# Optimization experiments

Hardware: AMD Instinct MI355X
Metric: run time of the kernel (lower is better)

## Reference

```python
import jax, jax.numpy as jnp
import numpy as np

N, C, H, W = 2, 128, 64, 64
N_HEAD = 4
GROUPS = 16
EPS = 1e-5


def group_norm(x, scale, offset):
    # haiku GroupNorm, channels_first: normalize over (channels-in-group, h, w)
    n, c, h, w = x.shape
    xg = x.reshape(n, GROUPS, c // GROUPS, h, w)
    mu = xg.mean(axis=(2, 3, 4), keepdims=True)
    var = xg.var(axis=(2, 3, 4), keepdims=True)
    xg = (xg - mu) * jax.lax.rsqrt(var + EPS)
    return xg.reshape(n, c, h, w) * scale[None, :, None, None] + offset[None, :, None, None]


def setup_inputs() -> dict:
    key = jax.random.key(0)
    ks = jax.random.split(key, 4)
    inv_sqrt_c = 1.0 / np.sqrt(C).astype(np.float32)
    return {
        "x": jax.random.normal(ks[0], (N, C, H, W), dtype=jnp.float32),
        "w_qkv": jax.random.normal(ks[1], (C, 3 * C), dtype=jnp.float32) * inv_sqrt_c,
        "b_qkv": jnp.zeros((3 * C,), dtype=jnp.float32),
        "w_out": jax.random.normal(ks[2], (C, C), dtype=jnp.float32) * inv_sqrt_c,
        "b_out": jnp.zeros((C,), dtype=jnp.float32),
        "gn1_scale": jnp.ones((C,), dtype=jnp.float32),
        "gn1_offset": jnp.zeros((C,), dtype=jnp.float32),
        "gn2_scale": jnp.ones((C,), dtype=jnp.float32),
        "gn2_offset": jnp.zeros((C,), dtype=jnp.float32),
    }


def reference(x, w_qkv, b_qkv, w_out, b_out, gn1_scale, gn1_offset, gn2_scale, gn2_offset):
    n, c, h, w = x.shape
    dh = c // N_HEAD
    # GroupNorm (x is reassigned, so the residual uses the normalized x)
    xn = group_norm(x, gn1_scale, gn1_offset)
    # 1x1 conv qkv projection: [n, 3c, h, w]
    qkv = jnp.einsum('nchw,cd->ndhw', xn, w_qkv) + b_qkv[None, :, None, None]
    # [n, 3H, dh, hw] -> [n, 3H, hw, dh]
    qkv = jnp.swapaxes(qkv.reshape(n, N_HEAD * 3, dh, h * w), 2, 3)
    q, k, v = jnp.split(qkv, 3, axis=1)  # each [n, H, hw, dh]
    scale = dh ** (-0.25)
    # [n, H, hw, hw] attention matrix (the memory-bound core)
    att = jax.nn.softmax((q * scale) @ (jnp.swapaxes(k, 2, 3) * scale), axis=3)
    y = jnp.swapaxes(att @ v, 2, 3).reshape(n, c, h, w)
    # 1x1 conv out projection + GroupNorm + residual
    out = jnp.einsum('nchw,cd->ndhw', y, w_out) + b_out[None, :, None, None]
    return xn + group_norm(out, gn2_scale, gn2_offset)
```

## Files before the change

kernel.cpp:

```cpp
#include <hip/hip_runtime.h>
#include <hip/hip_bf16.h>
#include <math.h>

constexpr int cHW   = 4096;
constexpr int cC    = 128;
constexpr int cNH   = 4;
constexpr int cDH   = 32;
constexpr float cEPS = 1e-5f;
constexpr float cQS = 0.2550347805f;
constexpr int SPLIT = 4;

typedef short bh8 __attribute__((ext_vector_type(8)));
typedef float f4  __attribute__((ext_vector_type(4)));

static __device__ __forceinline__ unsigned short f2bf(float f) {
  union { __hip_bfloat16 h; unsigned short u; } cv;
  cv.h = __float2bfloat16(f);
  return cv.u;
}
static __device__ __forceinline__ unsigned pack2bf(float a, float b) {
  return (unsigned)f2bf(a) | ((unsigned)f2bf(b) << 16);
}
static __device__ __forceinline__ unsigned pack_trunc(float a, float b) {
  unsigned ua = __builtin_bit_cast(unsigned, a);
  unsigned ub = __builtin_bit_cast(unsigned, b);
  return (ua >> 16) | (ub & 0xffff0000u);
}
static __device__ __forceinline__ float bflo(unsigned pk) {
  return __builtin_bit_cast(float, pk << 16);
}
static __device__ __forceinline__ float bfhi(unsigned pk) {
  return __builtin_bit_cast(float, pk & 0xffff0000u);
}

__device__ __forceinline__ void block_reduce2(float& a, float& b, float* sbuf) {
  #pragma unroll
  for (int off = 32; off > 0; off >>= 1) {
    a += __shfl_down(a, off, 64);
    b += __shfl_down(b, off, 64);
  }
  int wave = threadIdx.x >> 6;
  int lane = threadIdx.x & 63;
  if (lane == 0) { sbuf[wave] = a; sbuf[4 + wave] = b; }
  __syncthreads();
  if (threadIdx.x == 0) {
    sbuf[8] = sbuf[0] + sbuf[1] + sbuf[2] + sbuf[3];
    sbuf[9] = sbuf[4] + sbuf[5] + sbuf[6] + sbuf[7];
  }
  __syncthreads();
  a = sbuf[8];
  b = sbuf[9];
}

__global__ __launch_bounds__(256)
void prep(const float* __restrict__ x, float* __restrict__ part,
          const float* __restrict__ wq, const float* __restrict__ wo,
          unsigned short* __restrict__ wqT, unsigned short* __restrict__ woT) {
  __shared__ float lds[32 * 133];
  int L = threadIdx.x;
  if (blockIdx.x < 256) {
    int ng = blockIdx.x >> 3, sl = blockIdx.x & 7;
    const float4* s4 = (const float4*)x;
    float s = 0.f, s2 = 0.f;
    #pragma unroll
    for (int i = 0; i < 4; i++) {
      int idx = i * 256 + L;
      int c = idx >> 7, tt = idx & 127;
      float4 v = s4[(size_t)(ng * 8 + c) * 1024 + sl * 128 + tt];
      s  += v.x + v.y + v.z + v.w;
      s2 += v.x*v.x + v.y*v.y + v.z*v.z + v.w*v.w;
    }
    block_reduce2(s, s2, lds);
    if (L == 0) { part[blockIdx.x * 2] = s; part[blockIdx.x * 2 + 1] = s2; }
  } else {
    int bx = blockIdx.x - 256;
    const float* src; unsigned short* dst; int W, d0;
    if (bx < 12) { src = wq; dst = wqT; W = 384; d0 = bx * 32; }
    else         { src = wo; dst = woT; W = 128; d0 = (bx - 12) * 32; }
    #pragma unroll
    for (int i = 0; i < 16; i++) {
      int c = i * 8 + (L >> 5), d = L & 31;
      lds[d * 133 + c] = src[(size_t)c * W + d0 + d];
    }
    __syncthreads();
    int d = L >> 3, ch = L & 7, c0 = ch * 16;
    unsigned pk[8];
    #pragma unroll
    for (int j = 0; j < 8; j++)
      pk[j] = pack2bf(lds[d * 133 + c0 + 2 * j], lds[d * 133 + c0 + 2 * j + 1]);
    uint4* d4 = (uint4*)(dst + (size_t)(d0 + d) * 128 + c0);
    d4[0] = make_uint4(pk[0], pk[1], pk[2], pk[3]);
    d4[1] = make_uint4(pk[4], pk[5], pk[6], pk[7]);
  }
}

__global__ __launch_bounds__(256)
void gn_stats(const float* __restrict__ src, float* __restrict__ part) {
  __shared__ float sbuf[10];
  int ng = blockIdx.x >> 3, sl = blockIdx.x & 7;
  const float4* s4 = (const float4*)src;
  float s = 0.f, s2 = 0.f;
  #pragma unroll
  for (int i = 0; i < 4; i++) {
    int idx = i * 256 + threadIdx.x;
    int c = idx >> 7, tt = idx & 127;
    float4 v = s4[(size_t)(ng * 8 + c) * 1024 + sl * 128 + tt];
    s  += v.x + v.y + v.z + v.w;
    s2 += v.x*v.x + v.y*v.y + v.z*v.z + v.w*v.w;
  }
  block_reduce2(s, s2, sbuf);
  if (threadIdx.x == 0) { part[blockIdx.x * 2] = s; part[blockIdx.x * 2 + 1] = s2; }
}

__global__ __launch_bounds__(256)
void gn1_pack(const float* __restrict__ x, const float* __restrict__ part,
              const float* __restrict__ sc, const float* __restrict__ of,
              unsigned short* __restrict__ xnB) {
  int cc = blockIdx.x, ts = blockIdx.y, n = blockIdx.z;
  int ng = n * 16 + cc;
  float s = 0.f, s2 = 0.f;
  #pragma unroll
  for (int p = 0; p < 8; p++) { s += part[(ng*8+p)*2]; s2 += part[(ng*8+p)*2+1]; }
  float mu = s * (1.0f / 32768.0f);
  float rinv = rsqrtf(s2 * (1.0f / 32768.0f) - mu * mu + cEPS);
  int t = ts * 256 + threadIdx.x;
  float v[8];
  #pragma unroll
  for (int j = 0; j < 8; j++) {
    int c = cc * 8 + j;
    float a = rinv * sc[c];
    float bo = of[c] - mu * a;
    v[j] = x[((size_t)n * cC + c) * cHW + t] * a + bo;
  }
  unsigned pk[4];
  #pragma unroll
  for (int j = 0; j < 4; j++) pk[j] = pack2bf(v[2*j], v[2*j+1]);
  ((uint4*)xnB)[(size_t)(n * 16 + cc) * cHW + t] = make_uint4(pk[0], pk[1], pk[2], pk[3]);
}

__global__ __launch_bounds__(256)
void qkv_mfma(const unsigned short* __restrict__ xnB, const unsigned short* __restrict__ wqT,
              const float* __restrict__ bq, unsigned* __restrict__ qB,
              unsigned* __restrict__ kB, unsigned* __restrict__ vI) {
  __shared__ float vbuf[64 * 36];
  const int L = threadIdx.x & 63, w = threadIdx.x >> 6;
  const int c16 = L & 15, q = L >> 4;
  const int t0 = blockIdx.x * 64, dg = blockIdx.y, n = blockIdx.z;
  const int nh = n * 4 + (dg & 3), d0 = dg * 32;
  const f4 zf = {0.f, 0.f, 0.f, 0.f};
  f4 acc0 = zf, acc1 = zf;
  const int trow = t0 + w * 16 + c16;
  #pragma unroll
  for (int ks = 0; ks < 4; ks++) {
    bh8 a  = *(const bh8*)(xnB + ((size_t)(n * 16 + ks * 4 + q) * cHW + trow) * 8);
    bh8 b0 = *(const bh8*)(wqT + (size_t)(d0 + c16) * 128 + ks * 32 + q * 8);
    bh8 b1 = *(const bh8*)(wqT + (size_t)(d0 + 16 + c16) * 128 + ks * 32 + q * 8);
    acc0 = __builtin_amdgcn_mfma_f32_16x16x32_bf16(a, b0, acc0, 0, 0, 0);
    acc1 = __builtin_amdgcn_mfma_f32_16x16x32_bf16(a, b1, acc1, 0, 0, 0);
  }
  float blo = bq[d0 + c16], bhi = bq[d0 + 16 + c16];
  if (dg < 8) {
    float scl = (dg < 4) ? cQS : 1.0f;
    unsigned* dst = (dg < 4) ? qB : kB;
    #pragma unroll
    for (int r = 0; r < 4; r++) {
      unsigned pk = pack2bf((acc0[r] + blo) * scl, (acc1[r] + bhi) * scl);
      dst[((size_t)nh * cHW + t0 + w * 16 + q * 4 + r) * 16 + c16] = pk;
    }
  } else {
    #pragma unroll
    for (int r = 0; r < 4; r++) {
      vbuf[(w * 16 + q * 4 + r) * 36 + c16]      = acc0[r] + blo;
      vbuf[(w * 16 + q * 4 + r) * 36 + 16 + c16] = acc1[r] + bhi;
    }
    __syncthreads();
    int t16 = threadIdx.x & 15, dh8 = (threadIdx.x >> 4) & 15;
    #pragma unroll
    for (int blk = 0; blk < 2; blk++)
      #pragma unroll
      for (int hh = 0; hh < 2; hh++) {
        int dh = dh8 + hh * 16;
        float lo = vbuf[(blk * 32 + t16) * 36 + dh];
        float hi = vbuf[(blk * 32 + 16 + t16) * 36 + dh];
        vI[((size_t)nh * 32 + dh) * 2048 + (size_t)(t0 / 32 + blk) * 16 + t16] = pack2bf(lo, hi);
      }
  }
}

__global__ __launch_bounds__(256)
void flash_mfma(const unsigned short* __restrict__ qB,
                const unsigned short* __restrict__ kB,
                const unsigned short* __restrict__ vI,
                unsigned* __restrict__ opart, float* __restrict__ lpart) {
  __shared__ float pbuf[4][1280];
  const int w = threadIdx.x >> 6, L = threadIdx.x & 63;
  const int c16 = L & 15, q = L >> 4;
  const int qt = blockIdx.x * 4 + w, nh = blockIdx.y, ph = blockIdx.z;
  float* pb = pbuf[w];
  const f4 zf = {0.f, 0.f, 0.f, 0.f};
  const short oneb = 0x3F80;
  const bh8 ones = {oneb, oneb, oneb, oneb, oneb, oneb, oneb, oneb};

  const unsigned short* qb = qB + ((size_t)nh * cHW + qt * 32) * cDH;
  bh8 qa[2];
  qa[0] = *(const bh8*)(qb + (size_t)c16 * cDH + q * 8);
  qa[1] = *(const bh8*)(qb + (size_t)(16 + c16) * cDH + q * 8);

  f4 o[2][2] = {{zf, zf}, {zf, zf}};
  f4 lacc[2] = {zf, zf};

  const unsigned short* kb = kB + (size_t)nh * cHW * cDH;
  const unsigned short* vb = vI + (size_t)nh * cDH * cHW;

  const int kbeg = ph * (cHW / SPLIT);
  const int kend = kbeg + cHW / SPLIT;

  for (int kt = kbeg; kt < kend; kt += 64) {
    bh8 kf[4];
    #pragma unroll
    for (int s = 0; s < 4; s++)
      kf[s] = *(const bh8*)(kb + (size_t)(kt + s*16 + c16) * cDH + q * 8);
    bh8 vf[2][2];
    #pragma unroll
    for (int ks = 0; ks < 2; ks++)
      #pragma unroll
      for (int dt = 0; dt < 2; dt++)
        vf[ks][dt] = *(const bh8*)(vb + (size_t)(dt*16 + c16) * cHW + kt + ks*32 + q*8);

    f4 sf[2][4];
    #pragma unroll
    for (int rt = 0; rt < 2; rt++)
      #pragma unroll
      for (int s = 0; s < 4; s++)
        sf[rt][s] = __builtin_amdgcn_mfma_f32_16x16x32_bf16(qa[rt], kf[s], zf, 0, 0, 0);

    #pragma unroll
    for (int rt = 0; rt < 2; rt++) {
      #pragma unroll
      for (int s = 0; s < 4; s++)
        #pragma unroll
        for (int r = 0; r < 4; r++)
          sf[rt][s][r] = __builtin_amdgcn_exp2f(sf[rt][s][r]);
      #pragma unroll
      for (int st = 0; st < 2; st++)
        #pragma unroll
        for (int r = 0; r < 4; r++) {
          unsigned pk = pack_trunc(sf[rt][2*st][r], sf[rt][2*st+1][r]);
          pb[(rt*2 + st)*320 + (q*4 + r)*20 + c16] = __builtin_bit_cast(float, pk);
        }
    }
    #pragma unroll
    for (int rt = 0; rt < 2; rt++)
      #pragma unroll
      for (int st = 0; st < 2; st++) {
        bh8 pa = *(const bh8*)(pb + (rt*2 + st)*320 + c16*20 + q*4);
        o[rt][0] = __builtin_amdgcn_mfma_f32_16x16x32_bf16(pa, vf[st][0], o[rt][0], 0, 0, 0);
        o[rt][1] = __builtin_amdgcn_mfma_f32_16x16x32_bf16(pa, vf[st][1], o[rt][1], 0, 0, 0);
        lacc[rt] = __builtin_amdgcn_mfma_f32_16x16x32_bf16(pa, ones, lacc[rt], 0, 0, 0);
      }
  }

  size_t base_r = (size_t)ph * 32768 + (size_t)nh * cHW + (size_t)qt * 32;
  #pragma unroll
  for (int rt = 0; rt < 2; rt++)
    #pragma unroll
    for (int r = 0; r < 4; r++) {
      size_t rr = base_r + rt*16 + q*4 + r;
      if (c16 == 0) lpart[rr] = lacc[rt][r];
      opart[rr * 16 + c16] = pack_trunc(o[rt][0][r], o[rt][1][r]);
    }
}

__global__ __launch_bounds__(256)
void combine(const unsigned* __restrict__ opart, const float* __restrict__ lpart,
             unsigned* __restrict__ yB) {
  size_t r = (size_t)blockIdx.x * 256 + threadIdx.x;
  float l = 0.f;
  #pragma unroll
  for (int p = 0; p < SPLIT; p++) l += lpart[(size_t)p * 32768 + r];
  float e[32];
  #pragma unroll
  for (int j = 0; j < 32; j++) e[j] = 0.f;
  #pragma unroll
  for (int p = 0; p < SPLIT; p++) {
    const uint4* op = (const uint4*)(opart + ((size_t)p * 32768 + r) * 16);
    #pragma unroll
    for (int j = 0; j < 4; j++) {
      uint4 v = op[j];
      e[j*4+0] += bflo(v.x); e[16+j*4+0] += bfhi(v.x);
      e[j*4+1] += bflo(v.y); e[16+j*4+1] += bfhi(v.y);
      e[j*4+2] += bflo(v.z); e[16+j*4+2] += bfhi(v.z);
      e[j*4+3] += bflo(v.w); e[16+j*4+3] += bfhi(v.w);
    }
  }
  float inv = 1.0f / l;
  unsigned pk[16];
  #pragma unroll
  for (int m = 0; m < 16; m++) pk[m] = pack2bf(e[2*m] * inv, e[2*m+1] * inv);
  uint4* dst = (uint4*)(yB + r * 16);
  #pragma unroll
  for (int j = 0; j < 4; j++)
    dst[j] = make_uint4(pk[4*j], pk[4*j+1], pk[4*j+2], pk[4*j+3]);
}

__global__ __launch_bounds__(256)
void out_mfma(const unsigned short* __restrict__ yB, const unsigned short* __restrict__ woT,
              const float* __restrict__ bo, float* __restrict__ proj) {
  __shared__ float obuf[64 * 36];
  const int L = threadIdx.x & 63, w = threadIdx.x >> 6;
  const int c16 = L & 15, q = L >> 4;
  const int t0 = blockIdx.x * 64, d0 = blockIdx.y * 32, n = blockIdx.z;
  const f4 zf = {0.f, 0.f, 0.f, 0.f};
  f4 acc0 = zf, acc1 = zf;
  const int trow = t0 + w * 16 + c16;
  #pragma unroll
  for (int h = 0; h < 4; h++) {
    bh8 a  = *(const bh8*)(yB + ((size_t)(n * 4 + h) * cHW + trow) * 32 + q * 8);
    bh8 b0 = *(const bh8*)(woT + (size_t)(d0 + c16) * 128 + h * 32 + q * 8);
    bh8 b1 = *(const bh8*)(woT + (size_t)(d0 + 16 + c16) * 128 + h * 32 + q * 8);
    acc0 = __builtin_amdgcn_mfma_f32_16x16x32_bf16(a, b0, acc0, 0, 0, 0);
    acc1 = __builtin_amdgcn_mfma_f32_16x16x32_bf16(a, b1, acc1, 0, 0, 0);
  }
  float blo = bo[d0 + c16], bhi = bo[d0 + 16 + c16];
  #pragma unroll
  for (int r = 0; r < 4; r++) {
    obuf[(w * 16 + q * 4 + r) * 36 + c16]      = acc0[r] + blo;
    obuf[(w * 16 + q * 4 + r) * 36 + 16 + c16] = acc1[r] + bhi;
  }
  __syncthreads();
  int t16 = threadIdx.x & 15, d8 = (threadIdx.x >> 4) & 15;
  #pragma unroll
  for (int tc = 0; tc < 4; tc++)
    #pragma unroll
    for (int hh = 0; hh < 2; hh++) {
      int d = d8 + hh * 16;
      proj[((size_t)n * cC + d0 + d) * cHW + t0 + tc * 16 + t16] =
          obuf[(tc * 16 + t16) * 36 + d];
    }
}

__global__ __launch_bounds__(256)
void gn2_apply(const float* __restrict__ x, const float* __restrict__ proj,
               const float* __restrict__ p1, const float* __restrict__ p2,
               const float* __restrict__ s1, const float* __restrict__ o1,
               const float* __restrict__ s2, const float* __restrict__ o2,
               float* __restrict__ out) {
  int tid = blockIdx.x * 256 + threadIdx.x;
  int Cg = tid >> 8;
  int n = Cg >> 7, ch = Cg & 127, g = ch >> 3, ng = n * 16 + g;
  float sa = 0.f, sb = 0.f, ta = 0.f, tb = 0.f;
  #pragma unroll
  for (int p = 0; p < 8; p++) {
    sa += p1[(ng*8+p)*2]; sb += p1[(ng*8+p)*2+1];
    ta += p2[(ng*8+p)*2]; tb += p2[(ng*8+p)*2+1];
  }
  float mu1 = sa * (1.0f/32768.0f);
  float ri1 = rsqrtf(sb * (1.0f/32768.0f) - mu1*mu1 + cEPS);
  float a1 = ri1 * s1[ch], b1 = o1[ch] - mu1 * a1;
  float mu2 = ta * (1.0f/32768.0f);
  float ri2 = rsqrtf(tb * (1.0f/32768.0f) - mu2*mu2 + cEPS);
  float a2 = ri2 * s2[ch], b2 = o2[ch] - mu2 * a2;
  const float4* x4 = (const float4*)x;
  const float4* pr4 = (const float4*)proj;
  float4* o4 = (float4*)out;
  #pragma unroll
  for (int i = 0; i < 4; i++) {
    size_t f = (size_t)tid * 4 + i;
    float4 xv = x4[f], pv = pr4[f];
    float4 r;
    r.x = xv.x * a1 + b1 + pv.x * a2 + b2;
    r.y = xv.y * a1 + b1 + pv.y * a2 + b2;
    r.z = xv.z * a1 + b1 + pv.z * a2 + b2;
    r.w = xv.w * a1 + b1 + pv.w * a2 + b2;
    o4[f] = r;
  }
}

extern "C" void kernel_launch(void* const* d_in, const int* in_sizes, int n_in,
                              void* d_out, int out_size, void* d_ws, size_t ws_size,
                              hipStream_t stream) {
  const float* x     = (const float*)d_in[0];
  const float* w_qkv = (const float*)d_in[1];
  const float* b_qkv = (const float*)d_in[2];
  const float* w_out = (const float*)d_in[3];
  const float* b_out = (const float*)d_in[4];
  const float* g1s   = (const float*)d_in[5];
  const float* g1o   = (const float*)d_in[6];
  const float* g2s   = (const float*)d_in[7];
  const float* g2o   = (const float*)d_in[8];
  float* out = (float*)d_out;
  float* ws  = (float*)d_ws;

  const size_t MAP = (size_t)2 * cC * cHW;
  float* proj    = ws;
  float* lpart   = proj + MAP;
  float* stats1  = lpart + (size_t)SPLIT * 32768;
  float* stats2  = stats1 + 512;
  unsigned* opart = (unsigned*)(stats2 + 512);
  unsigned* qB   = opart + (size_t)SPLIT * 32768 * 16;
  unsigned* kB   = qB + MAP / 2;
  unsigned* vI   = kB + MAP / 2;
  unsigned* yB   = vI + MAP / 2;
  unsigned short* xnB = (unsigned short*)(yB + MAP / 2);
  unsigned short* wqT = xnB + MAP;
  unsigned short* woT = wqT + 49152;

  prep      <<<dim3(272),           256, 0, stream>>>(x, stats1, w_qkv, w_out, wqT, woT);
  gn1_pack  <<<dim3(16, 16, 2),     256, 0, stream>>>(x, stats1, g1s, g1o, xnB);
  qkv_mfma  <<<dim3(64, 12, 2),     256, 0, stream>>>(xnB, wqT, b_qkv, qB, kB, vI);
  flash_mfma<<<dim3(32, 8, SPLIT),  256, 0, stream>>>((const unsigned short*)qB,
                                                      (const unsigned short*)kB,
                                                      (const unsigned short*)vI,
                                                      opart, lpart);
  combine   <<<dim3(128),           256, 0, stream>>>(opart, lpart, yB);
  out_mfma  <<<dim3(64, 4, 2),      256, 0, stream>>>((const unsigned short*)yB, woT,
                                                      b_out, proj);
  gn_stats  <<<dim3(256),           256, 0, stream>>>(proj, stats2);
  gn2_apply <<<dim3(256),           256, 0, stream>>>(x, proj, stats1, stats2,
                                                      g1s, g1o, g2s, g2o, out);
}
```

Measured before the change: 149.0 us.

## Switch flash attention to 32x32 MFMA with permlane swaps instead of LDS

The attention kernel now uses 32x32x16 bf16 MFMA tiles and computes S transposed (K as the A operand, Q as B). The exponentiated scores are repacked into the PV operand layout with v_permlane32_swap in registers, which removes the per-wave LDS staging buffer and its round trip. The V interleave order and the combine kernel's output layout are changed to match the new accumulator row mapping, and launch bounds now request occupancy 4. This trades LDS traffic and extra instructions for register shuffles, and it depends on the new row/column mapping being exactly right.

```diff
diff --git a/kernel.cpp b/kernel.cpp
--- a/kernel.cpp
+++ b/kernel.cpp
@@ -10,8 +10,9 @@
 constexpr float cQS = 0.2550347805f;
 constexpr int SPLIT = 4;
 
-typedef short bh8 __attribute__((ext_vector_type(8)));
-typedef float f4  __attribute__((ext_vector_type(4)));
+typedef short bh8  __attribute__((ext_vector_type(8)));
+typedef float f4   __attribute__((ext_vector_type(4)));
+typedef float f16a __attribute__((ext_vector_type(16)));
 
 static __device__ __forceinline__ unsigned short f2bf(float f) {
   union { __hip_bfloat16 h; unsigned short u; } cv;
@@ -31,6 +32,20 @@
 }
 static __device__ __forceinline__ float bfhi(unsigned pk) {
   return __builtin_bit_cast(float, pk & 0xffff0000u);
+}
+static __device__ __forceinline__ void plswap(unsigned& a, unsigned& b) {
+#if __has_builtin(__builtin_amdgcn_permlane32_swap)
+  typedef int v2i __attribute__((ext_vector_type(2)));
+  v2i r = __builtin_amdgcn_permlane32_swap((int)a, (int)b, false, false);
+  a = (unsigned)r[0]; b = (unsigned)r[1];
+#else
+  asm("v_permlane32_swap_b32 %0, %1" : "+v"(a), "+v"(b));
+#endif
+}
+static __device__ __forceinline__ bh8 mk8(unsigned a, unsigned b, unsigned c, unsigned d) {
+  union { unsigned u[4]; bh8 v; } t;
+  t.u[0] = a; t.u[1] = b; t.u[2] = c; t.u[3] = d;
+  return t.v;
 }
 
 __device__ __forceinline__ void block_reduce2(float& a, float& b, float* sbuf) {
@@ -180,127 +195,123 @@
       #pragma unroll
       for (int hh = 0; hh < 2; hh++) {
         int dh = dh8 + hh * 16;
-        float lo = vbuf[(blk * 32 + t16) * 36 + dh];
-        float hi = vbuf[(blk * 32 + 16 + t16) * 36 + dh];
+        float lo = vbuf[(blk * 32 + 2 * t16) * 36 + dh];
+        float hi = vbuf[(blk * 32 + 2 * t16 + 1) * 36 + dh];
         vI[((size_t)nh * 32 + dh) * 2048 + (size_t)(t0 / 32 + blk) * 16 + t16] = pack2bf(lo, hi);
       }
   }
 }
 
-__global__ __launch_bounds__(256)
+__global__ __launch_bounds__(256, 4)
 void flash_mfma(const unsigned short* __restrict__ qB,
                 const unsigned short* __restrict__ kB,
                 const unsigned short* __restrict__ vI,
                 unsigned* __restrict__ opart, float* __restrict__ lpart) {
-  __shared__ float pbuf[4][1280];
   const int w = threadIdx.x >> 6, L = threadIdx.x & 63;
-  const int c16 = L & 15, q = L >> 4;
+  const int col = L & 31, hi = L >> 5;
   const int qt = blockIdx.x * 4 + w, nh = blockIdx.y, ph = blockIdx.z;
-  float* pb = pbuf[w];
-  const f4 zf = {0.f, 0.f, 0.f, 0.f};
   const short oneb = 0x3F80;
   const bh8 ones = {oneb, oneb, oneb, oneb, oneb, oneb, oneb, oneb};
-
-  const unsigned short* qb = qB + ((size_t)nh * cHW + qt * 32) * cDH;
-  bh8 qa[2];
-  qa[0] = *(const bh8*)(qb + (size_t)c16 * cDH + q * 8);
-  qa[1] = *(const bh8*)(qb + (size_t)(16 + c16) * cDH + q * 8);
-
-  f4 o[2][2] = {{zf, zf}, {zf, zf}};
-  f4 lacc[2] = {zf, zf};
+  const f16a zf16 = {0.f,0.f,0.f,0.f, 0.f,0.f,0.f,0.f, 0.f,0.f,0.f,0.f, 0.f,0.f,0.f,0.f};
+
+  const unsigned short* qb = qB + ((size_t)nh * cHW + (size_t)qt * 32) * cDH;
+  bh8 qf0 = *(const bh8*)(qb + (size_t)col * cDH + hi * 8);
+  bh8 qf1 = *(const bh8*)(qb + (size_t)col * cDH + 16 + hi * 8);
 
   const unsigned short* kb = kB + (size_t)nh * cHW * cDH;
-  const unsigned short* vb = vI + (size_t)nh * cDH * cHW;
+  const unsigned short* vb = vI + (size_t)nh * cDH * cHW + (size_t)col * cHW + hi * 8;
+
+  f16a o = zf16, lacc = zf16;
 
   const int kbeg = ph * (cHW / SPLIT);
   const int kend = kbeg + cHW / SPLIT;
 
   for (int kt = kbeg; kt < kend; kt += 64) {
-    bh8 kf[4];
-    #pragma unroll
-    for (int s = 0; s < 4; s++)
-      kf[s] = *(const bh8*)(kb + (size_t)(kt + s*16 + c16) * cDH + q * 8);
-    bh8 vf[2][2];
-    #pragma unroll
-    for (int ks = 0; ks < 2; ks++)
+    #pragma unroll
+    for (int st = 0; st < 2; st++) {
+      const int ktb = kt + st * 32;
+      bh8 vfa = *(const bh8*)(vb + ktb);
+      bh8 vfb = *(const bh8*)(vb + ktb + 16);
+      const unsigned short* krow = kb + (size_t)(ktb + col) * cDH;
+      bh8 ka0 = *(const bh8*)(krow + hi * 8);
+      bh8 ka1 = *(const bh8*)(krow + 16 + hi * 8);
+      f16a s = __builtin_amdgcn_mfma_f32_32x32x16_bf16(ka0, qf0, zf16, 0, 0, 0);
+      s = __builtin_amdgcn_mfma_f32_32x32x16_bf16(ka1, qf1, s, 0, 0, 0);
       #pragma unroll
-      for (int dt = 0; dt < 2; dt++)
-        vf[ks][dt] = *(const bh8*)(vb + (size_t)(dt*16 + c16) * cHW + kt + ks*32 + q*8);
-
-    f4 sf[2][4];
-    #pragma unroll
-    for (int rt = 0; rt < 2; rt++)
-      #pragma unroll
-      for (int s = 0; s < 4; s++)
-        sf[rt][s] = __builtin_amdgcn_mfma_f32_16x16x32_bf16(qa[rt], kf[s], zf, 0, 0, 0);
-
-    #pragma unroll
-    for (int rt = 0; rt < 2; rt++) {
-      #pragma unroll
-      for (int s = 0; s < 4; s++)
-        #pragma unroll
-        for (int r = 0; r < 4; r++)
-          sf[rt][s][r] = __builtin_amdgcn_exp2f(sf[rt][s][r]);
-      #pragma unroll
-      for (int st = 0; st < 2; st++)
-        #pragma unroll
-        for (int r = 0; r < 4; r++) {
-          unsigned pk = pack_trunc(sf[rt][2*st][r], sf[rt][2*st+1][r]);
-          pb[(rt*2 + st)*320 + (q*4 + r)*20 + c16] = __builtin_bit_cast(float, pk);
-        }
-    }
-    #pragma unroll
-    for (int rt = 0; rt < 2; rt++)
-      #pragma unroll
-      for (int st = 0; st < 2; st++) {
-        bh8 pa = *(const bh8*)(pb + (rt*2 + st)*320 + c16*20 + q*4);
-        o[rt][0] = __builtin_amdgcn_mfma_f32_16x16x32_bf16(pa, vf[st][0], o[rt][0], 0, 0, 0);
-        o[rt][1] = __builtin_amdgcn_mfma_f32_16x16x32_bf16(pa, vf[st][1], o[rt][1], 0, 0, 0);
-        lacc[rt] = __builtin_amdgcn_mfma_f32_16x16x32_bf16(pa, ones, lacc[rt], 0, 0, 0);
-      }
-  }
-
-  size_t base_r = (size_t)ph * 32768 + (size_t)nh * cHW + (size_t)qt * 32;
-  #pragma unroll
-  for (int rt = 0; rt < 2; rt++)
-    #pragma unroll
-    for (int r = 0; r < 4; r++) {
-      size_t rr = base_r + rt*16 + q*4 + r;
-      if (c16 == 0) lpart[rr] = lacc[rt][r];
-      opart[rr * 16 + c16] = pack_trunc(o[rt][0][r], o[rt][1][r]);
-    }
+      for (int r = 0; r < 16; r++) s[r] = __builtin_amdgcn_exp2f(s[r]);
+      unsigned pk0 = pack_trunc(s[0],  s[1]);
+      unsigned pk1 = pack_trunc(s[2],  s[3]);
+      unsigned pk2 = pack_trunc(s[4],  s[5]);
+      unsigned pk3 = pack_trunc(s[6],  s[7]);
+      unsigned pk4 = pack_trunc(s[8],  s[9]);
+      unsigned pk5 = pack_trunc(s[10], s[11]);
+      unsigned pk6 = pack_trunc(s[12], s[13]);
+      unsigned pk7 = pack_trunc(s[14], s[15]);
+      plswap(pk0, pk2); plswap(pk1, pk3);
+      plswap(pk4, pk6); plswap(pk5, pk7);
+      bh8 pf0 = mk8(pk0, pk1, pk2, pk3);
+      bh8 pf1 = mk8(pk4, pk5, pk6, pk7);
+      o    = __builtin_amdgcn_mfma_f32_32x32x16_bf16(pf0, vfa,  o,    0, 0, 0);
+      lacc = __builtin_amdgcn_mfma_f32_32x32x16_bf16(pf0, ones, lacc, 0, 0, 0);
+      o    = __builtin_amdgcn_mfma_f32_32x32x16_bf16(pf1, vfb,  o,    0, 0, 0);
+      lacc = __builtin_amdgcn_mfma_f32_32x32x16_bf16(pf1, ones, lacc, 0, 0, 0);
+    }
+  }
+
+  const size_t base = (size_t)ph * 32768 + (size_t)nh * cHW + (size_t)qt * 32;
+  #pragma unroll
+  for (int k = 0; k < 8; k++) {
+    const int rowlo = ((2 * k) & 3) + 8 * (k >> 1) + 4 * hi;
+    opart[((base + rowlo) >> 1) * 32 + col] = pack_trunc(o[2 * k], o[2 * k + 1]);
+  }
+  if (col == 0) {
+    #pragma unroll
+    for (int r = 0; r < 16; r++)
+      lpart[base + (r & 3) + 8 * (r >> 2) + 4 * hi] = lacc[r];
+  }
 }
 
 __global__ __launch_bounds__(256)
 void combine(const unsigned* __restrict__ opart, const float* __restrict__ lpart,
              unsigned* __restrict__ yB) {
-  size_t r = (size_t)blockIdx.x * 256 + threadIdx.x;
-  float l = 0.f;
-  #pragma unroll
-  for (int p = 0; p < SPLIT; p++) l += lpart[(size_t)p * 32768 + r];
-  float e[32];
-  #pragma unroll
-  for (int j = 0; j < 32; j++) e[j] = 0.f;
+  int tid = blockIdx.x * 256 + threadIdx.x;
+  size_t rp = (size_t)(tid >> 1);
+  int h = tid & 1;
+  size_t r0 = rp * 2;
+  float l0 = 0.f, l1 = 0.f;
   #pragma unroll
   for (int p = 0; p < SPLIT; p++) {
-    const uint4* op = (const uint4*)(opart + ((size_t)p * 32768 + r) * 16);
+    l0 += lpart[(size_t)p * 32768 + r0];
+    l1 += lpart[(size_t)p * 32768 + r0 + 1];
+  }
+  float e0[16], e1[16];
+  #pragma unroll
+  for (int j = 0; j < 16; j++) { e0[j] = 0.f; e1[j] = 0.f; }
+  #pragma unroll
+  for (int p = 0; p < SPLIT; p++) {
+    const uint4* op = (const uint4*)(opart + ((size_t)p * 16384 + rp) * 32 + h * 16);
     #pragma unroll
     for (int j = 0; j < 4; j++) {
       uint4 v = op[j];
-      e[j*4+0] += bflo(v.x); e[16+j*4+0] += bfhi(v.x);
-      e[j*4+1] += bflo(v.y); e[16+j*4+1] += bfhi(v.y);
-      e[j*4+2] += bflo(v.z); e[16+j*4+2] += bfhi(v.z);
-      e[j*4+3] += bflo(v.w); e[16+j*4+3] += bfhi(v.w);
-    }
-  }
-  float inv = 1.0f / l;
-  unsigned pk[16];
-  #pragma unroll
-  for (int m = 0; m < 16; m++) pk[m] = pack2bf(e[2*m] * inv, e[2*m+1] * inv);
-  uint4* dst = (uint4*)(yB + r * 16);
-  #pragma unroll
-  for (int j = 0; j < 4; j++)
-    dst[j] = make_uint4(pk[4*j], pk[4*j+1], pk[4*j+2], pk[4*j+3]);
+      e0[j*4+0] += bflo(v.x); e1[j*4+0] += bfhi(v.x);
+      e0[j*4+1] += bflo(v.y); e1[j*4+1] += bfhi(v.y);
+      e0[j*4+2] += bflo(v.z); e1[j*4+2] += bfhi(v.z);
+      e0[j*4+3] += bflo(v.w); e1[j*4+3] += bfhi(v.w);
+    }
+  }
+  float i0 = 1.0f / l0, i1 = 1.0f / l1;
+  unsigned pkA[8], pkB[8];
+  #pragma unroll
+  for (int j = 0; j < 8; j++) {
+    pkA[j] = pack2bf(e0[2*j] * i0, e0[2*j+1] * i0);
+    pkB[j] = pack2bf(e1[2*j] * i1, e1[2*j+1] * i1);
+  }
+  uint4* dA = (uint4*)(yB + r0 * 16 + h * 8);
+  dA[0] = make_uint4(pkA[0], pkA[1], pkA[2], pkA[3]);
+  dA[1] = make_uint4(pkA[4], pkA[5], pkA[6], pkA[7]);
+  uint4* dB = (uint4*)(yB + (r0 + 1) * 16 + h * 8);
+  dB[0] = make_uint4(pkB[0], pkB[1], pkB[2], pkB[3]);
+  dB[1] = make_uint4(pkB[4], pkB[5], pkB[6], pkB[7]);
 }
 
 __global__ __launch_bounds__(256)
```

After: 148.8 us. Within noise of the previous version (-0.1%).
